# Performance work log

Hardware: AMD Instinct MI355X
Metric: run time of the kernel (lower is better)

## Reference

```python
import jax, jax.numpy as jnp
import numpy as np

# ---- model hyperparameters (from init_kwargs) ----
PATTERN_SPECS = ((6, 50), (5, 50), (4, 50), (3, 50))  # (pattern_len, num_patterns)
MAX_LEN = max(pl for pl, _ in PATTERN_SPECS)          # 6
P = sum(n for _, n in PATTERN_SPECS)                  # 200 total patterns
LM1 = MAX_LEN - 1                                     # 5 transitions per pattern
EMB_DIM = 300
N_LOCAL = 10000
BIAS_SCALE = 1.0
TAU = 0.0
LN_EPS = 1e-5
NEG_INF = -jnp.inf
# end state (index into hidden dim of size MAX_LEN) per pattern
END_STATES = jnp.asarray([pl - 1 for pl, n in PATTERN_SPECS for _ in range(n)], dtype=jnp.int32)  # [P]


def setup_inputs() -> dict:
    key = jax.random.key(0)
    ks = jax.random.split(key, 8)
    B, T = 128, 256
    local_embeddings = jax.random.normal(ks[0], (EMB_DIM, N_LOCAL), jnp.float32)
    diags = jax.random.normal(ks[1], (P * LM1, EMB_DIM), jnp.float32) * 0.05   # xavier-ish
    bias = jax.random.normal(ks[2], (P * LM1, 1), jnp.float32) * 0.05
    wildcards = jax.random.normal(ks[3], (P, LM1), jnp.float32) * 0.05
    linear_w = jax.random.normal(ks[4], (2, P), jnp.float32) * 0.05
    linear_b = jax.random.normal(ks[5], (2,), jnp.float32) * 0.05
    docs = jax.random.randint(ks[6], (B, T), 0, N_LOCAL, dtype=jnp.int32)
    doc_lens = jax.random.randint(ks[7], (B,), MAX_LEN - 1, T + 1, dtype=jnp.int32)
    return {"local_embeddings": local_embeddings, "diags": diags, "bias": bias,
            "wildcards": wildcards, "linear_w": linear_w, "linear_b": linear_b,
            "docs": docs, "doc_lens": doc_lens}


def reference(local_embeddings, diags, bias, wildcards, linear_w, linear_b, docs, doc_lens):
    # Max-sum semiring: times=add, plus=max, one=0, zero=-inf, outer maps = identity.
    B, T = docs.shape
    # transition scores for every local-vocab token: [N_LOCAL, P*LM1]
    trans = (jnp.matmul(diags, local_embeddings) + BIAS_SCALE * bias).T
    tm = trans[docs].reshape(B, T, P, LM1)            # [B,T,P,LM1]
    wc = wildcards                                     # wildcard_scale = one = 0 under max-sum
    restart = jnp.zeros((B, P, 1), trans.dtype)        # semiring.one
    hid0 = jnp.concatenate([jnp.zeros((B, P, 1), trans.dtype),
                            jnp.full((B, P, LM1), NEG_INF, trans.dtype)], axis=2)  # [B,P,MAX_LEN]
    scores0 = jnp.full((B, P), NEG_INF, trans.dtype)
    active = (jnp.arange(T)[None, :] < doc_lens[:, None]).T  # [T,B]

    def step(carry, xt):
        hid, sc = carry
        tm_t, m_t = xt                                 # [B,P,LM1], [B]
        prev = hid[:, :, :-1]
        new = jnp.maximum(prev + tm_t, prev + wc[None])   # main vs wildcard transition
        hid = jnp.concatenate([restart, new], axis=2)
        endv = jnp.take_along_axis(hid, END_STATES[None, :, None].astype(jnp.int32), axis=2)[..., 0]  # [B,P]
        sc = jnp.where(m_t[:, None], jnp.maximum(sc, endv), sc)
        return (hid, sc), None

    (_, scores), _ = jax.lax.scan(step, (hid0, scores0), (jnp.transpose(tm, (1, 0, 2, 3)), active))

    # replace never-completed patterns (-inf) with the per-row min of finite scores
    neg_mask = scores == NEG_INF
    s = jnp.where(neg_mask, jnp.inf, scores)
    row_min = jnp.min(s, axis=1, keepdims=True)
    s = jnp.where(jnp.isinf(s), row_min, s)
    # LayerNorm without affine
    mu = jnp.mean(s, axis=-1, keepdims=True)
    var = jnp.var(s, axis=-1, keepdims=True)
    s = (s - mu) / jnp.sqrt(var + LN_EPS)
    # STE binarizer forward
    s = (s > TAU).astype(trans.dtype)
    # final linear
    return jnp.matmul(s, linear_w.T) + linear_b
```

## Files before the change

kernel.cpp:

```cpp
#include <hip/hip_runtime.h>
#include <math.h>

#define EMB   300
#define NLOC  10000
#define PP    200
#define NN    1000
#define BB    128
#define TT    256
#define NSEG  8
#define SEGLEN 32

#define NVBLK 79
#define NNBLK 8
#define NKPAN 40
#define ASCALE 16.f
#define BSCALE 64.f
#define OUTSCALE (1.f / 1024.f)

typedef _Float16 f16x8 __attribute__((ext_vector_type(8)));
typedef float    f32x4 __attribute__((ext_vector_type(4)));

__global__ __launch_bounds__(128) void split_a(const float* __restrict__ emb,
                                               _Float16* __restrict__ Ah,
                                               _Float16* __restrict__ Al) {
    const int m    = threadIdx.x;
    const int vblk = blockIdx.x;
    const int kpan = blockIdx.y;
    const int v    = vblk * 128 + m;
    const size_t outb = ((size_t)(vblk * NKPAN + kpan) * 128 + m) * 8;
    _Float16 hi[8], lo[8];
    #pragma unroll
    for (int j = 0; j < 8; ++j) {
        int e = kpan * 8 + j;
        float x = (v < NLOC && e < EMB) ? emb[(size_t)e * NLOC + v] : 0.f;
        float xs = ASCALE * x;
        _Float16 h = (_Float16)xs;
        hi[j] = h;
        lo[j] = (_Float16)(xs - (float)h);
    }
    *(f16x8*)&Ah[outb] = *(const f16x8*)hi;
    *(f16x8*)&Al[outb] = *(const f16x8*)lo;
}

__global__ __launch_bounds__(128) void split_b(const float* __restrict__ diags,
                                               _Float16* __restrict__ Bh,
                                               _Float16* __restrict__ Bl) {
    const int nn   = threadIdx.x;
    const int nblk = blockIdx.x;
    const int kpan = blockIdx.y;
    const int n    = nblk * 128 + nn;
    const size_t outb = ((size_t)(nblk * NKPAN + kpan) * 128 + nn) * 8;
    _Float16 hi[8], lo[8];
    #pragma unroll
    for (int j = 0; j < 8; ++j) {
        int e = kpan * 8 + j;
        float x = (n < NN && e < EMB) ? diags[(size_t)n * EMB + e] : 0.f;
        float xs = BSCALE * x;
        _Float16 h = (_Float16)xs;
        hi[j] = h;
        lo[j] = (_Float16)(xs - (float)h);
    }
    *(f16x8*)&Bh[outb] = *(const f16x8*)hi;
    *(f16x8*)&Bl[outb] = *(const f16x8*)lo;
}

__global__ __launch_bounds__(256, 2) void gemm_s1(
    const _Float16* __restrict__ Ah, const _Float16* __restrict__ Al,
    const _Float16* __restrict__ Bh, const _Float16* __restrict__ Bl,
    const float* __restrict__ bias, float* __restrict__ trans, int tstr) {
    const int tid  = threadIdx.x;

    const int bid  = blockIdx.x;
    const int swz  = (bid & 7) * 79 + (bid >> 3);
    const int vblk = swz >> 3;
    const int nblk = swz & 7;

    const int lane = tid & 63;
    const int wave = tid >> 6;
    const int wr   = wave >> 1;
    const int wc   = wave & 1;
    const int l15  = lane & 15;
    const int hh   = lane >> 4;

    const size_t aoff = (size_t)vblk * (NKPAN * 1024) + (size_t)hh * 1024 + (size_t)(wr * 64 + l15) * 8;
    const size_t boff = (size_t)nblk * (NKPAN * 1024) + (size_t)hh * 1024 + (size_t)(wc * 64 + l15) * 8;
    const _Float16* pAh = Ah + aoff;
    const _Float16* pAl = Al + aoff;
    const _Float16* pBh = Bh + boff;
    const _Float16* pBl = Bl + boff;

    f32x4 acc[4][4] = {};

    #pragma unroll
    for (int s = 0; s < 10; ++s) {
        f16x8 fah[4], fal[4], fbh[4], fbl[4];
        #pragma unroll
        for (int i = 0; i < 4; ++i) {
            fah[i] = *(const f16x8*)(pAh + s * 4096 + i * 128);
            fal[i] = *(const f16x8*)(pAl + s * 4096 + i * 128);
            fbh[i] = *(const f16x8*)(pBh + s * 4096 + i * 128);
            fbl[i] = *(const f16x8*)(pBl + s * 4096 + i * 128);
        }
        #pragma unroll
        for (int i = 0; i < 4; ++i)
            #pragma unroll
            for (int j = 0; j < 4; ++j) {
                acc[i][j] = __builtin_amdgcn_mfma_f32_16x16x32_f16(fah[i], fbh[j], acc[i][j], 0, 0, 0);
                acc[i][j] = __builtin_amdgcn_mfma_f32_16x16x32_f16(fah[i], fbl[j], acc[i][j], 0, 0, 0);
                acc[i][j] = __builtin_amdgcn_mfma_f32_16x16x32_f16(fal[i], fbh[j], acc[i][j], 0, 0, 0);
            }
    }

    __shared__ float etile[64][132];

    #pragma unroll 1
    for (int h = 0; h < 2; ++h) {
        __syncthreads();
        if (wr == h) {
            #pragma unroll
            for (int i = 0; i < 4; ++i)
                #pragma unroll
                for (int j = 0; j < 4; ++j)
                    #pragma unroll
                    for (int r = 0; r < 4; ++r)
                        etile[i * 16 + hh * 4 + r][wc * 64 + j * 16 + l15] =
                            acc[i][j][r] * OUTSCALE;
        }
        __syncthreads();
        #pragma unroll
        for (int it = 0; it < 8; ++it) {
            const int idx = it * 256 + tid;
            const int row = idx >> 5;
            const int c4  = (idx & 31) * 4;
            const int v   = vblk * 128 + h * 64 + row;
            const int n   = nblk * 128 + c4;
            if (v < NLOC && n + 3 < NN) {
                float4 val = *(const float4*)&etile[row][c4];
                const float4 b4 = *(const float4*)&bias[n];
                val.x += b4.x; val.y += b4.y; val.z += b4.z; val.w += b4.w;
                *(float4*)&trans[(size_t)v * tstr + n] = val;
            }
        }
    }
}

__global__ __launch_bounds__(256) void trans_gemm(const float* __restrict__ emb,
                                                  const float* __restrict__ diags,
                                                  const float* __restrict__ bias,
                                                  float* __restrict__ trans) {
    const int tid = threadIdx.x;
    const int tn  = tid & 15;
    const int tv  = tid >> 4;
    const int v0  = blockIdx.x * 128;
    const int n0  = blockIdx.y * 128;
    __shared__ float As[15][132];
    __shared__ float Bs[15][132];
    float acc[8][8] = {};
    for (int kk = 0; kk < 20; ++kk) {
        const int e0 = kk * 15;
        #pragma unroll
        for (int l = tid; l < 480; l += 256) {
            int k = l >> 5, c = l & 31;
            int v = v0 + c * 4;
            const float* src = emb + (size_t)(e0 + k) * NLOC + v;
            float4 val;
            if (v + 3 < NLOC) val = *(const float4*)src;
            else {
                val.x = (v + 0 < NLOC) ? src[0] : 0.f;
                val.y = (v + 1 < NLOC) ? src[1] : 0.f;
                val.z = (v + 2 < NLOC) ? src[2] : 0.f;
                val.w = (v + 3 < NLOC) ? src[3] : 0.f;
            }
            *(float4*)&As[k][c * 4] = val;
        }
        for (int l = tid; l < 1920; l += 256) {
            int nn = l / 15, k = l - nn * 15;
            int n = n0 + nn;
            Bs[k][nn] = (n < NN) ? diags[n * EMB + e0 + k] : 0.f;
        }
        __syncthreads();
        #pragma unroll
        for (int k = 0; k < 15; ++k) {
            float4 a0 = *(const float4*)&As[k][tv * 4];
            float4 a1 = *(const float4*)&As[k][tv * 4 + 64];
            float4 b0 = *(const float4*)&Bs[k][tn * 4];
            float4 b1 = *(const float4*)&Bs[k][tn * 4 + 64];
            float av[8] = {a0.x, a0.y, a0.z, a0.w, a1.x, a1.y, a1.z, a1.w};
            float bv[8] = {b0.x, b0.y, b0.z, b0.w, b1.x, b1.y, b1.z, b1.w};
            #pragma unroll
            for (int i = 0; i < 8; ++i)
                #pragma unroll
                for (int j = 0; j < 8; ++j)
                    acc[i][j] += av[i] * bv[j];
        }
        __syncthreads();
    }
    #pragma unroll
    for (int i = 0; i < 8; ++i) {
        int v = v0 + (i >> 2) * 64 + tv * 4 + (i & 3);
        if (v >= NLOC) continue;
        #pragma unroll
        for (int jh = 0; jh < 2; ++jh) {
            int n = n0 + jh * 64 + tn * 4;
            if (n + 3 < NN) {
                float4 r;
                r.x = acc[i][jh * 4 + 0] + bias[n + 0];
                r.y = acc[i][jh * 4 + 1] + bias[n + 1];
                r.z = acc[i][jh * 4 + 2] + bias[n + 2];
                r.w = acc[i][jh * 4 + 3] + bias[n + 3];
                *(float4*)&trans[(size_t)v * NN + n] = r;
            } else {
                #pragma unroll
                for (int j = 0; j < 4; ++j)
                    if (n + j < NN)
                        trans[(size_t)v * NN + n + j] = acc[i][jh * 4 + j] + bias[n + j];
            }
        }
    }
}

__global__ __launch_bounds__(256) void scan_seg(const float* __restrict__ trans,
                                                const float* __restrict__ wildcards,
                                                const int* __restrict__ docs,
                                                const int* __restrict__ doc_lens,
                                                float* __restrict__ partial, int tstr) {
    const int b   = blockIdx.x;
    const int seg = blockIdx.y;
    const int tid = threadIdx.x;
    __shared__ int sdoc[TT];
    sdoc[tid] = docs[b * TT + tid];
    __syncthreads();

    const bool act = tid < PP;
    const int  p   = act ? tid : (PP - 1);
    const int  p5  = p * 5;
    const int  len = doc_lens[b];
    const int  t0  = seg * SEGLEN;
    const int  start = (t0 - 4 > 0) ? t0 - 4 : 0;
    const int  end   = (t0 + SEGLEN < len) ? t0 + SEGLEN : len;

    const float NI = -INFINITY;
    float score = NI;

    if (start < end) {
        const float w0 = wildcards[p5 + 0];
        const float w1 = wildcards[p5 + 1];
        const float w2 = wildcards[p5 + 2];
        const float w3 = wildcards[p5 + 3];
        const float w4 = wildcards[p5 + 4];
        const int e = (p < 50) ? 5 : (p < 100) ? 4 : (p < 150) ? 3 : 2;

        float h1 = NI, h2 = NI, h3 = NI, h4 = NI, h5 = NI;
        const int nt   = end - start;
        const int ntm1 = nt - 1;

        float A[5], B[5], C[5];
#define LOADR(R, idx) { int tt = (idx); tt = (tt < ntm1) ? tt : ntm1;          \
        const float* r_ = trans + (size_t)sdoc[start + tt] * tstr + p5;        \
        R[0] = r_[0]; R[1] = r_[1]; R[2] = r_[2]; R[3] = r_[3]; R[4] = r_[4]; }
#define STEP(R, t) { \
        float u0 = fmaxf(R[0], w0), u1 = fmaxf(R[1], w1), u2 = fmaxf(R[2], w2);\
        float u3 = fmaxf(R[3], w3), u4 = fmaxf(R[4], w4);                      \
        h5 = h4 + u4; h4 = h3 + u3; h3 = h2 + u2; h2 = h1 + u1; h1 = u0;       \
        if ((t) >= t0) {                                                       \
            float endv = (e == 5) ? h5 : (e == 4) ? h4 : (e == 3) ? h3 : h2;   \
            score = fmaxf(score, endv);                                        \
        } }

        LOADR(A, 0); LOADR(B, 1); LOADR(C, 2);
        for (int i = 0; i < nt; i += 3) {
            STEP(A, start + i);
            LOADR(A, i + 3);
            if (i + 1 < nt) { STEP(B, start + i + 1); }
            LOADR(B, i + 4);
            if (i + 2 < nt) { STEP(C, start + i + 2); }
            LOADR(C, i + 5);
        }
#undef LOADR
#undef STEP
    }

    if (act) partial[((size_t)b * NSEG + seg) * PP + p] = score;
}

__device__ inline float block_sum_bcast(float v, volatile float* red, int tid) {
    #pragma unroll
    for (int o = 32; o > 0; o >>= 1) v += __shfl_down(v, o, 64);
    __syncthreads();
    if ((tid & 63) == 0) red[tid >> 6] = v;
    __syncthreads();
    return red[0] + red[1] + red[2] + red[3];
}

__global__ __launch_bounds__(256) void finalize(const float* __restrict__ partial,
                                                const float* __restrict__ linear_w,
                                                const float* __restrict__ linear_b,
                                                float* __restrict__ out) {
    const int b   = blockIdx.x;
    const int tid = threadIdx.x;
    __shared__ float red[4];

    const bool act = tid < PP;
    const int  p   = act ? tid : (PP - 1);

    float m = -INFINITY;
    #pragma unroll
    for (int s = 0; s < NSEG; ++s)
        m = fmaxf(m, partial[((size_t)b * NSEG + s) * PP + p]);

    float total = block_sum_bcast(act ? m : 0.f, red, tid);
    float mu = total * (1.f / (float)PP);

    int bin = (act && m > mu) ? 1 : 0;
    float c0 = bin ? linear_w[p]      : 0.f;
    float c1 = bin ? linear_w[PP + p] : 0.f;

    float r0 = block_sum_bcast(c0, red, tid);
    float r1 = block_sum_bcast(c1, red, tid);

    if (tid == 0) {
        out[b * 2 + 0] = r0 + linear_b[0];
        out[b * 2 + 1] = r1 + linear_b[1];
    }
}

extern "C" void kernel_launch(void* const* d_in, const int* in_sizes, int n_in,
                              void* d_out, int out_size, void* d_ws, size_t ws_size,
                              hipStream_t stream) {
    const float* emb    = (const float*)d_in[0];
    const float* diags  = (const float*)d_in[1];
    const float* bias   = (const float*)d_in[2];
    const float* wc     = (const float*)d_in[3];
    const float* lw     = (const float*)d_in[4];
    const float* lb     = (const float*)d_in[5];
    const int*   docs   = (const int*)d_in[6];
    const int*   dlens  = (const int*)d_in[7];
    float*       out    = (float*)d_out;

    const size_t aElems = (size_t)NVBLK * NKPAN * 128 * 8;
    const size_t bElems = (size_t)NNBLK * NKPAN * 128 * 8;
    const size_t partialElems = (size_t)BB * NSEG * PP;
    const size_t f16Bytes = (2 * aElems + 2 * bElems) * sizeof(_Float16);

    int tstr;
    {
        const size_t need1024 = ((size_t)NLOC * 1024 + partialElems) * 4 + f16Bytes;
        const size_t need1000 = ((size_t)NLOC * 1000 + partialElems) * 4 + f16Bytes;
        if (ws_size >= need1024)       tstr = 1024;
        else if (ws_size >= need1000)  tstr = 1000;
        else                           tstr = 0;
    }

    float* trans   = (float*)d_ws;
    float* partial = trans + (size_t)NLOC * (tstr ? tstr : 1000);
    _Float16* Ah = (_Float16*)(partial + partialElems);
    _Float16* Al = Ah + aElems;
    _Float16* Bh = Al + aElems;
    _Float16* Bl = Bh + bElems;

    if (tstr) {
        split_a<<<dim3(NVBLK, NKPAN, 1), 128, 0, stream>>>(emb, Ah, Al);
        split_b<<<dim3(NNBLK, NKPAN, 1), 128, 0, stream>>>(diags, Bh, Bl);
        gemm_s1<<<dim3(NVBLK * NNBLK, 1, 1), 256, 0, stream>>>(Ah, Al, Bh, Bl, bias, trans, tstr);
        scan_seg<<<dim3(BB, NSEG, 1), 256, 0, stream>>>(trans, wc, docs, dlens, partial, tstr);
    } else {
        trans_gemm<<<dim3(79, 8, 1), 256, 0, stream>>>(emb, diags, bias, trans);
        scan_seg<<<dim3(BB, NSEG, 1), 256, 0, stream>>>(trans, wc, docs, dlens, partial, 1000);
    }
    finalize<<<BB, 256, 0, stream>>>(partial, lw, lb, out);
}
```

Baseline: 56.49 us.

## Stage GEMM operands through LDS via global_load_lds and merge split kernels

The two fp16 split kernels are merged into one launch, removing a kernel launch. The split-fp16 GEMM now stages each K-slab of A/B hi/lo panels into shared memory with direct global-to-LDS loads, so each tile is fetched once per block and shared between waves instead of every wave reading its fragments from global memory. Occupancy is raised to 3 blocks per SIMD and the staging buffer is unioned with the epilogue tile. In exchange, the K-loop is no longer unrolled and there is no double buffering, so each slab adds two barriers with no overlap between loads and MFMA.

```diff
diff --git a/kernel.cpp b/kernel.cpp
--- a/kernel.cpp
+++ b/kernel.cpp
@@ -20,54 +20,61 @@
 typedef _Float16 f16x8 __attribute__((ext_vector_type(8)));
 typedef float    f32x4 __attribute__((ext_vector_type(4)));
 
-__global__ __launch_bounds__(128) void split_a(const float* __restrict__ emb,
-                                               _Float16* __restrict__ Ah,
-                                               _Float16* __restrict__ Al) {
+typedef const __attribute__((address_space(1))) unsigned int GUI;
+typedef __attribute__((address_space(3))) unsigned int LUI;
+
+__global__ __launch_bounds__(128) void split_ab(const float* __restrict__ emb,
+                                                const float* __restrict__ diags,
+                                                _Float16* __restrict__ Ah,
+                                                _Float16* __restrict__ Al,
+                                                _Float16* __restrict__ Bh,
+                                                _Float16* __restrict__ Bl) {
     const int m    = threadIdx.x;
-    const int vblk = blockIdx.x;
+    const int bx   = blockIdx.x;
     const int kpan = blockIdx.y;
-    const int v    = vblk * 128 + m;
-    const size_t outb = ((size_t)(vblk * NKPAN + kpan) * 128 + m) * 8;
     _Float16 hi[8], lo[8];
-    #pragma unroll
-    for (int j = 0; j < 8; ++j) {
-        int e = kpan * 8 + j;
-        float x = (v < NLOC && e < EMB) ? emb[(size_t)e * NLOC + v] : 0.f;
-        float xs = ASCALE * x;
-        _Float16 h = (_Float16)xs;
-        hi[j] = h;
-        lo[j] = (_Float16)(xs - (float)h);
-    }
-    *(f16x8*)&Ah[outb] = *(const f16x8*)hi;
-    *(f16x8*)&Al[outb] = *(const f16x8*)lo;
-}
-
-__global__ __launch_bounds__(128) void split_b(const float* __restrict__ diags,
-                                               _Float16* __restrict__ Bh,
-                                               _Float16* __restrict__ Bl) {
-    const int nn   = threadIdx.x;
-    const int nblk = blockIdx.x;
-    const int kpan = blockIdx.y;
-    const int n    = nblk * 128 + nn;
-    const size_t outb = ((size_t)(nblk * NKPAN + kpan) * 128 + nn) * 8;
-    _Float16 hi[8], lo[8];
-    #pragma unroll
-    for (int j = 0; j < 8; ++j) {
-        int e = kpan * 8 + j;
-        float x = (n < NN && e < EMB) ? diags[(size_t)n * EMB + e] : 0.f;
-        float xs = BSCALE * x;
-        _Float16 h = (_Float16)xs;
-        hi[j] = h;
-        lo[j] = (_Float16)(xs - (float)h);
-    }
-    *(f16x8*)&Bh[outb] = *(const f16x8*)hi;
-    *(f16x8*)&Bl[outb] = *(const f16x8*)lo;
-}
-
-__global__ __launch_bounds__(256, 2) void gemm_s1(
+    if (bx < NVBLK) {
+        const int vblk = bx;
+        const int v    = vblk * 128 + m;
+        const size_t outb = ((size_t)(vblk * NKPAN + kpan) * 128 + m) * 8;
+        #pragma unroll
+        for (int j = 0; j < 8; ++j) {
+            int e = kpan * 8 + j;
+            float x = (v < NLOC && e < EMB) ? emb[(size_t)e * NLOC + v] : 0.f;
+            float xs = ASCALE * x;
+            _Float16 h = (_Float16)xs;
+            hi[j] = h;
+            lo[j] = (_Float16)(xs - (float)h);
+        }
+        *(f16x8*)&Ah[outb] = *(const f16x8*)hi;
+        *(f16x8*)&Al[outb] = *(const f16x8*)lo;
+    } else {
+        const int nblk = bx - NVBLK;
+        const int n    = nblk * 128 + m;
+        const size_t outb = ((size_t)(nblk * NKPAN + kpan) * 128 + m) * 8;
+        #pragma unroll
+        for (int j = 0; j < 8; ++j) {
+            int e = kpan * 8 + j;
+            float x = (n < NN && e < EMB) ? diags[(size_t)n * EMB + e] : 0.f;
+            float xs = BSCALE * x;
+            _Float16 h = (_Float16)xs;
+            hi[j] = h;
+            lo[j] = (_Float16)(xs - (float)h);
+        }
+        *(f16x8*)&Bh[outb] = *(const f16x8*)hi;
+        *(f16x8*)&Bl[outb] = *(const f16x8*)lo;
+    }
+}
+
+__global__ __launch_bounds__(256, 3) void gemm_lds(
     const _Float16* __restrict__ Ah, const _Float16* __restrict__ Al,
     const _Float16* __restrict__ Bh, const _Float16* __restrict__ Bl,
     const float* __restrict__ bias, float* __restrict__ trans, int tstr) {
+    __shared__ union {
+        _Float16 stage[4][4096];
+        float    etile[64][132];
+    } sh;
+
     const int tid  = threadIdx.x;
 
     const int bid  = blockIdx.x;
@@ -82,36 +89,47 @@
     const int l15  = lane & 15;
     const int hh   = lane >> 4;
 
-    const size_t aoff = (size_t)vblk * (NKPAN * 1024) + (size_t)hh * 1024 + (size_t)(wr * 64 + l15) * 8;
-    const size_t boff = (size_t)nblk * (NKPAN * 1024) + (size_t)hh * 1024 + (size_t)(wc * 64 + l15) * 8;
-    const _Float16* pAh = Ah + aoff;
-    const _Float16* pAl = Al + aoff;
-    const _Float16* pBh = Bh + boff;
-    const _Float16* pBl = Bl + boff;
+    const _Float16* gsrc[4] = {
+        Ah + (size_t)vblk * (NKPAN * 1024),
+        Al + (size_t)vblk * (NKPAN * 1024),
+        Bh + (size_t)nblk * (NKPAN * 1024),
+        Bl + (size_t)nblk * (NKPAN * 1024)};
 
     f32x4 acc[4][4] = {};
 
-    #pragma unroll
     for (int s = 0; s < 10; ++s) {
-        f16x8 fah[4], fal[4], fbh[4], fbl[4];
-        #pragma unroll
-        for (int i = 0; i < 4; ++i) {
-            fah[i] = *(const f16x8*)(pAh + s * 4096 + i * 128);
-            fal[i] = *(const f16x8*)(pAl + s * 4096 + i * 128);
-            fbh[i] = *(const f16x8*)(pBh + s * 4096 + i * 128);
-            fbl[i] = *(const f16x8*)(pBl + s * 4096 + i * 128);
-        }
-        #pragma unroll
-        for (int i = 0; i < 4; ++i)
+        #pragma unroll
+        for (int L = 0; L < 8; ++L) {
+            const int arr = L >> 1;
+            const int off = ((L & 1) * 256 + tid) * 8;
+            __builtin_amdgcn_global_load_lds(
+                (GUI*)(gsrc[arr] + (size_t)s * 4096 + off),
+                (LUI*)&sh.stage[arr][off], 16, 0, 0);
+        }
+        __syncthreads();
+
+        {
+            f16x8 fah[4], fal[4], fbh[4], fbl[4];
             #pragma unroll
-            for (int j = 0; j < 4; ++j) {
-                acc[i][j] = __builtin_amdgcn_mfma_f32_16x16x32_f16(fah[i], fbh[j], acc[i][j], 0, 0, 0);
-                acc[i][j] = __builtin_amdgcn_mfma_f32_16x16x32_f16(fah[i], fbl[j], acc[i][j], 0, 0, 0);
-                acc[i][j] = __builtin_amdgcn_mfma_f32_16x16x32_f16(fal[i], fbh[j], acc[i][j], 0, 0, 0);
+            for (int i = 0; i < 4; ++i) {
+                const int ra = hh * 128 + wr * 64 + i * 16 + l15;
+                fah[i] = *(const f16x8*)&sh.stage[0][ra * 8];
+                fal[i] = *(const f16x8*)&sh.stage[1][ra * 8];
+                const int rb = hh * 128 + wc * 64 + i * 16 + l15;
+                fbh[i] = *(const f16x8*)&sh.stage[2][rb * 8];
+                fbl[i] = *(const f16x8*)&sh.stage[3][rb * 8];
             }
-    }
-
-    __shared__ float etile[64][132];
+            #pragma unroll
+            for (int i = 0; i < 4; ++i)
+                #pragma unroll
+                for (int j = 0; j < 4; ++j) {
+                    acc[i][j] = __builtin_amdgcn_mfma_f32_16x16x32_f16(fah[i], fbh[j], acc[i][j], 0, 0, 0);
+                    acc[i][j] = __builtin_amdgcn_mfma_f32_16x16x32_f16(fah[i], fbl[j], acc[i][j], 0, 0, 0);
+                    acc[i][j] = __builtin_amdgcn_mfma_f32_16x16x32_f16(fal[i], fbh[j], acc[i][j], 0, 0, 0);
+                }
+        }
+        __syncthreads();
+    }
 
     #pragma unroll 1
     for (int h = 0; h < 2; ++h) {
@@ -123,7 +141,7 @@
                 for (int j = 0; j < 4; ++j)
                     #pragma unroll
                     for (int r = 0; r < 4; ++r)
-                        etile[i * 16 + hh * 4 + r][wc * 64 + j * 16 + l15] =
+                        sh.etile[i * 16 + hh * 4 + r][wc * 64 + j * 16 + l15] =
                             acc[i][j][r] * OUTSCALE;
         }
         __syncthreads();
@@ -135,7 +153,7 @@
             const int v   = vblk * 128 + h * 64 + row;
             const int n   = nblk * 128 + c4;
             if (v < NLOC && n + 3 < NN) {
-                float4 val = *(const float4*)&etile[row][c4];
+                float4 val = *(const float4*)&sh.etile[row][c4];
                 const float4 b4 = *(const float4*)&bias[n];
                 val.x += b4.x; val.y += b4.y; val.z += b4.z; val.w += b4.w;
                 *(float4*)&trans[(size_t)v * tstr + n] = val;
@@ -359,9 +377,8 @@
     _Float16* Bl = Bh + bElems;
 
     if (tstr) {
-        split_a<<<dim3(NVBLK, NKPAN, 1), 128, 0, stream>>>(emb, Ah, Al);
-        split_b<<<dim3(NNBLK, NKPAN, 1), 128, 0, stream>>>(diags, Bh, Bl);
-        gemm_s1<<<dim3(NVBLK * NNBLK, 1, 1), 256, 0, stream>>>(Ah, Al, Bh, Bl, bias, trans, tstr);
+        split_ab<<<dim3(NVBLK + NNBLK, NKPAN, 1), 128, 0, stream>>>(emb, diags, Ah, Al, Bh, Bl);
+        gemm_lds<<<dim3(NVBLK * NNBLK, 1, 1), 256, 0, stream>>>(Ah, Al, Bh, Bl, bias, trans, tstr);
         scan_seg<<<dim3(BB, NSEG, 1), 256, 0, stream>>>(trans, wc, docs, dlens, partial, tstr);
     } else {
         trans_gemm<<<dim3(79, 8, 1), 256, 0, stream>>>(emb, diags, bias, trans);
```

Measured after the change: 68.34 us. +21.0%, slower.
